# Kernel tuning notes

Measured on AMD Instinct MI355X. Metric: run time of the kernel, lower is better.

## Reference

```python
import jax, jax.numpy as jnp
import numpy as np
import math

B, N, M, O = 64, 2048, 64, 128  # batch, neurons, in_dims, out_dims


def setup_inputs() -> dict:
    key = jax.random.key(0)
    kx, kw, kb = jax.random.split(key, 3)
    s = 1.0 / math.sqrt(M + O)
    x = jax.random.normal(kx, (B, N, M), dtype=jnp.float32)
    # master weights fp32, init U(-s, s) as in the torch module
    w1 = jax.random.uniform(kw, (M, O, N), dtype=jnp.float32, minval=-s, maxval=s)
    b1 = jnp.zeros((1, N, O), dtype=jnp.float32)
    return {"x": x, "w1": w1, "b1": b1}


def reference(x, w1, b1):
    # N independent per-neuron linears: [B,N,M] x [M,O,N] -> [B,N,O]
    # cast master weights/bias to compute dtype (matches .to(x.dtype))
    w = w1.astype(x.dtype)
    b = b1.astype(x.dtype)
    return jnp.einsum('bnm,mon->bno', x, w) + b
```

## Files before the change

kernel.cpp:

```cpp
#include <hip/hip_runtime.h>
#include <hip/hip_bf16.h>

#define N_TOT 2048
#define M_DIM 64
#define O_DIM 128
#define NT 8

typedef __bf16 bf16x8 __attribute__((ext_vector_type(8)));
typedef __bf16 bf16x4 __attribute__((ext_vector_type(4)));
typedef float f32x4 __attribute__((ext_vector_type(4)));

__global__ __launch_bounds__(1024, 4) void superlinear_mfma(
    const float* __restrict__ x, const float* __restrict__ w1,
    const float* __restrict__ b1, float* __restrict__ out)
{
    __shared__ unsigned char wlds[NT * O_DIM * M_DIM * 2];

    const int tid  = threadIdx.x;
    const int lane = tid & 63;
    const int wave = tid >> 6;

    const int bid  = blockIdx.x;
    const int nblk = (bid & 7) * 32 + (bid >> 3);
    const int n0   = nblk * NT;

    const int nn  = wave & 7;
    const int bh  = wave >> 3;
    const int n   = n0 + nn;
    const int col = lane & 15;
    const int kg  = lane >> 4;

    float4 xr[2][2][2];
    #pragma unroll
    for (int kc = 0; kc < 2; ++kc) {
        #pragma unroll
        for (int bt = 0; bt < 2; ++bt) {
            int b = bh * 32 + bt * 16 + col;
            const float* xp = x + ((size_t)b * N_TOT + n) * M_DIM + kc * 32 + kg * 8;
            xr[kc][bt][0] = *(const float4*)xp;
            xr[kc][bt][1] = *(const float4*)(xp + 4);
        }
    }
    float bv[8];
    #pragma unroll
    for (int ot = 0; ot < 8; ++ot)
        bv[ot] = b1[(size_t)n * O_DIM + ot * 16 + col];

    #pragma unroll
    for (int it = 0; it < 4; ++it) {
        int u  = it * 1024 + tid;
        int n4 = u & 1;
        int o  = (u >> 1) & 127;
        int mq = u >> 8;
        int m  = mq * 4;
        const float* gp = w1 + ((size_t)m * O_DIM + o) * N_TOT + n0 + n4 * 4;
        float4 r0 = *(const float4*)(gp);
        float4 r1 = *(const float4*)(gp + (size_t)O_DIM * N_TOT);
        float4 r2 = *(const float4*)(gp + (size_t)2 * O_DIM * N_TOT);
        float4 r3 = *(const float4*)(gp + (size_t)3 * O_DIM * N_TOT);
        const float* a0 = (const float*)&r0;
        const float* a1 = (const float*)&r1;
        const float* a2 = (const float*)&r2;
        const float* a3 = (const float*)&r3;
        #pragma unroll
        for (int j = 0; j < 4; ++j) {
            int nnw = n4 * 4 + j;
            bf16x4 pk;
            pk[0] = (__bf16)a0[j];
            pk[1] = (__bf16)a1[j];
            pk[2] = (__bf16)a2[j];
            pk[3] = (__bf16)a3[j];
            unsigned addr = (unsigned)(nnw * 16384 + o * 128 + m * 2);
            addr ^= (unsigned)((o & 7) << 4);
            *(bf16x4*)(wlds + addr) = pk;
        }
    }

    bf16x8 af[2][2];
    #pragma unroll
    for (int kc = 0; kc < 2; ++kc) {
        #pragma unroll
        for (int bt = 0; bt < 2; ++bt) {
            const float* lp = (const float*)&xr[kc][bt][0];
            const float* hp = (const float*)&xr[kc][bt][1];
            bf16x8 v;
            #pragma unroll
            for (int j = 0; j < 4; ++j) {
                v[j]     = (__bf16)lp[j];
                v[4 + j] = (__bf16)hp[j];
            }
            af[kc][bt] = v;
        }
    }

    __syncthreads();

    #pragma unroll
    for (int ot = 0; ot < 8; ++ot) {
        unsigned addr = (unsigned)(nn * 16384 + (ot * 16 + col) * 128 + kg * 16);
        addr ^= (unsigned)((col & 7) << 4);
        bf16x8 bf0 = *(const bf16x8*)(wlds + addr);
        bf16x8 bf1 = *(const bf16x8*)(wlds + (addr ^ 64u));
        f32x4 ci;
        ci[0] = bv[ot]; ci[1] = bv[ot]; ci[2] = bv[ot]; ci[3] = bv[ot];
        #pragma unroll
        for (int bt = 0; bt < 2; ++bt) {
            f32x4 a = __builtin_amdgcn_mfma_f32_16x16x32_bf16(af[0][bt], bf0, ci, 0, 0, 0);
            a       = __builtin_amdgcn_mfma_f32_16x16x32_bf16(af[1][bt], bf1, a,  0, 0, 0);
            #pragma unroll
            for (int r = 0; r < 4; ++r) {
                int b = bh * 32 + bt * 16 + kg * 4 + r;
                __builtin_nontemporal_store(
                    a[r], out + ((size_t)b * N_TOT + n) * O_DIM + ot * 16 + col);
            }
        }
    }
}

extern "C" void kernel_launch(void* const* d_in, const int* in_sizes, int n_in,
                              void* d_out, int out_size, void* d_ws, size_t ws_size,
                              hipStream_t stream) {
    const float* x  = (const float*)d_in[0];
    const float* w1 = (const float*)d_in[1];
    const float* b1 = (const float*)d_in[2];
    float* out = (float*)d_out;
    superlinear_mfma<<<dim3(256), dim3(1024), 0, stream>>>(x, w1, b1, out);
}
```

Measured before the change: 40.14 us.

## Pipeline weight staging per output tile with double-buffered LDS and 512-thread blocks

Blocks shrink from 1024 to 512 threads, with one wave per neuron covering all 64 batch rows, so each wave now does four batch tiles. Weights are no longer staged all at once into a 128 KB LDS buffer. They are loaded one 16-column output tile at a time into a double-buffered 32 KB LDS area, with the global loads for the next tile issued before the current tile's MFMAs. This aims to overlap weight fetch with compute and cut LDS use, at the cost of a barrier per tile and fewer threads per block. Output stores also switch from nontemporal to regular stores.

```diff
diff --git a/kernel.cpp b/kernel.cpp
--- a/kernel.cpp
+++ b/kernel.cpp
@@ -10,11 +10,11 @@
 typedef __bf16 bf16x4 __attribute__((ext_vector_type(4)));
 typedef float f32x4 __attribute__((ext_vector_type(4)));
 
-__global__ __launch_bounds__(1024, 4) void superlinear_mfma(
+__global__ __launch_bounds__(512, 2) void superlinear_mfma(
     const float* __restrict__ x, const float* __restrict__ w1,
     const float* __restrict__ b1, float* __restrict__ out)
 {
-    __shared__ unsigned char wlds[NT * O_DIM * M_DIM * 2];
+    __shared__ unsigned char wlds[2 * NT * 16 * M_DIM * 2];
 
     const int tid  = threadIdx.x;
     const int lane = tid & 63;
@@ -23,64 +23,71 @@
     const int bid  = blockIdx.x;
     const int nblk = (bid & 7) * 32 + (bid >> 3);
     const int n0   = nblk * NT;
+    const int n    = n0 + wave;
 
-    const int nn  = wave & 7;
-    const int bh  = wave >> 3;
-    const int n   = n0 + nn;
     const int col = lane & 15;
     const int kg  = lane >> 4;
 
-    float4 xr[2][2][2];
-    #pragma unroll
-    for (int kc = 0; kc < 2; ++kc) {
+    const int half = tid & 1;
+    const int ol   = (tid >> 1) & 15;
+    const int m4   = (tid >> 5) * 4;
+
+    const size_t MSTR = (size_t)O_DIM * N_TOT;
+
+    auto stage_issue = [&](int ot, float4* r) {
+        const float* gp = w1 + (size_t)m4 * MSTR + (size_t)(ot * 16 + ol) * N_TOT
+                             + n0 + half * 4;
+        r[0] = *(const float4*)gp;
+        r[1] = *(const float4*)(gp + MSTR);
+        r[2] = *(const float4*)(gp + 2 * MSTR);
+        r[3] = *(const float4*)(gp + 3 * MSTR);
+    };
+    auto stage_write = [&](int ot, const float4* r) {
+        unsigned base = (unsigned)(ot & 1) << 14;
+        const float* a0 = (const float*)&r[0];
+        const float* a1 = (const float*)&r[1];
+        const float* a2 = (const float*)&r[2];
+        const float* a3 = (const float*)&r[3];
         #pragma unroll
-        for (int bt = 0; bt < 2; ++bt) {
-            int b = bh * 32 + bt * 16 + col;
-            const float* xp = x + ((size_t)b * N_TOT + n) * M_DIM + kc * 32 + kg * 8;
-            xr[kc][bt][0] = *(const float4*)xp;
-            xr[kc][bt][1] = *(const float4*)(xp + 4);
+        for (int j = 0; j < 4; ++j) {
+            int nn = half * 4 + j;
+            bf16x4 pk;
+            pk[0] = (__bf16)a0[j];
+            pk[1] = (__bf16)a1[j];
+            pk[2] = (__bf16)a2[j];
+            pk[3] = (__bf16)a3[j];
+            unsigned addr = (unsigned)(nn * 2048 + ol * 128 + m4 * 2);
+            addr ^= (unsigned)((ol & 7) << 4);
+            *(bf16x4*)(wlds + base + addr) = pk;
         }
-    }
+    };
+
+    float4 sr[4];
+    stage_issue(0, sr);
+
     float bv[8];
     #pragma unroll
     for (int ot = 0; ot < 8; ++ot)
         bv[ot] = b1[(size_t)n * O_DIM + ot * 16 + col];
 
+    float4 xr[2][4][2];
     #pragma unroll
-    for (int it = 0; it < 4; ++it) {
-        int u  = it * 1024 + tid;
-        int n4 = u & 1;
-        int o  = (u >> 1) & 127;
-        int mq = u >> 8;
-        int m  = mq * 4;
-        const float* gp = w1 + ((size_t)m * O_DIM + o) * N_TOT + n0 + n4 * 4;
-        float4 r0 = *(const float4*)(gp);
-        float4 r1 = *(const float4*)(gp + (size_t)O_DIM * N_TOT);
-        float4 r2 = *(const float4*)(gp + (size_t)2 * O_DIM * N_TOT);
-        float4 r3 = *(const float4*)(gp + (size_t)3 * O_DIM * N_TOT);
-        const float* a0 = (const float*)&r0;
-        const float* a1 = (const float*)&r1;
-        const float* a2 = (const float*)&r2;
-        const float* a3 = (const float*)&r3;
+    for (int kc = 0; kc < 2; ++kc)
         #pragma unroll
-        for (int j = 0; j < 4; ++j) {
-            int nnw = n4 * 4 + j;
-            bf16x4 pk;
-            pk[0] = (__bf16)a0[j];
-            pk[1] = (__bf16)a1[j];
-            pk[2] = (__bf16)a2[j];
-            pk[3] = (__bf16)a3[j];
-            unsigned addr = (unsigned)(nnw * 16384 + o * 128 + m * 2);
-            addr ^= (unsigned)((o & 7) << 4);
-            *(bf16x4*)(wlds + addr) = pk;
+        for (int bt = 0; bt < 4; ++bt) {
+            int b = bt * 16 + col;
+            const float* xp = x + ((size_t)b * N_TOT + n) * M_DIM + kc * 32 + kg * 8;
+            xr[kc][bt][0] = *(const float4*)xp;
+            xr[kc][bt][1] = *(const float4*)(xp + 4);
         }
-    }
 
-    bf16x8 af[2][2];
+    stage_write(0, sr);
+
+    bf16x8 af[2][4];
     #pragma unroll
-    for (int kc = 0; kc < 2; ++kc) {
+    for (int kc = 0; kc < 2; ++kc)
         #pragma unroll
-        for (int bt = 0; bt < 2; ++bt) {
+        for (int bt = 0; bt < 4; ++bt) {
             const float* lp = (const float*)&xr[kc][bt][0];
             const float* hp = (const float*)&xr[kc][bt][1];
             bf16x8 v;
@@ -91,28 +98,45 @@
             }
             af[kc][bt] = v;
         }
-    }
 
-    __syncthreads();
+    asm volatile("s_waitcnt lgkmcnt(0)" ::: "memory");
+    __builtin_amdgcn_s_barrier();
+    __builtin_amdgcn_sched_barrier(0);
 
     #pragma unroll
     for (int ot = 0; ot < 8; ++ot) {
-        unsigned addr = (unsigned)(nn * 16384 + (ot * 16 + col) * 128 + kg * 16);
+        float4 srn[4];
+        if (ot < 7) stage_issue(ot + 1, srn);
+
+        unsigned base = (unsigned)(ot & 1) << 14;
+        unsigned addr = (unsigned)(wave * 2048 + col * 128 + kg * 16);
         addr ^= (unsigned)((col & 7) << 4);
-        bf16x8 bf0 = *(const bf16x8*)(wlds + addr);
-        bf16x8 bf1 = *(const bf16x8*)(wlds + (addr ^ 64u));
-        f32x4 ci;
-        ci[0] = bv[ot]; ci[1] = bv[ot]; ci[2] = bv[ot]; ci[3] = bv[ot];
+        bf16x8 bf0 = *(const bf16x8*)(wlds + base + addr);
+        bf16x8 bf1 = *(const bf16x8*)(wlds + base + (addr ^ 64u));
+
+        f32x4 a[4];
         #pragma unroll
-        for (int bt = 0; bt < 2; ++bt) {
-            f32x4 a = __builtin_amdgcn_mfma_f32_16x16x32_bf16(af[0][bt], bf0, ci, 0, 0, 0);
-            a       = __builtin_amdgcn_mfma_f32_16x16x32_bf16(af[1][bt], bf1, a,  0, 0, 0);
+        for (int bt = 0; bt < 4; ++bt) {
+            f32x4 ci;
+            ci[0] = bv[ot]; ci[1] = bv[ot]; ci[2] = bv[ot]; ci[3] = bv[ot];
+            a[bt] = __builtin_amdgcn_mfma_f32_16x16x32_bf16(af[0][bt], bf0, ci,    0, 0, 0);
+            a[bt] = __builtin_amdgcn_mfma_f32_16x16x32_bf16(af[1][bt], bf1, a[bt], 0, 0, 0);
+        }
+
+        if (ot < 7) stage_write(ot + 1, srn);
+
+        #pragma unroll
+        for (int bt = 0; bt < 4; ++bt)
             #pragma unroll
             for (int r = 0; r < 4; ++r) {
-                int b = bh * 32 + bt * 16 + kg * 4 + r;
-                __builtin_nontemporal_store(
-                    a[r], out + ((size_t)b * N_TOT + n) * O_DIM + ot * 16 + col);
+                int b = bt * 16 + kg * 4 + r;
+                out[((size_t)b * N_TOT + n) * O_DIM + ot * 16 + col] = a[bt][r];
             }
+
+        if (ot < 7) {
+            asm volatile("s_waitcnt lgkmcnt(0)" ::: "memory");
+            __builtin_amdgcn_s_barrier();
+            __builtin_amdgcn_sched_barrier(0);
         }
     }
 }
@@ -124,5 +148,5 @@
     const float* w1 = (const float*)d_in[1];
     const float* b1 = (const float*)d_in[2];
     float* out = (float*)d_out;
-    superlinear_mfma<<<dim3(256), dim3(1024), 0, stream>>>(x, w1, b1, out);
+    superlinear_mfma<<<dim3(256), dim3(512), 0, stream>>>(x, w1, b1, out);
 }
```

After: 35.70 us. -11.1%, faster.
